# Kernel optimization log

Measured on AMD Instinct MI355X. Metric: run time of the kernel, lower is better.

## Reference

```python
import jax, jax.numpy as jnp
import numpy as np

B, C, H, W = 8, 21, 512, 512
MAX_M = 0.5   # args.ldam_max_m
S = 30.0      # args.ldam_s


def setup_inputs() -> dict:
    key = jax.random.key(0)
    k1, k2 = jax.random.split(key)
    pred = jax.random.normal(k1, (B, C, H, W), dtype=jnp.float32)
    target = jax.random.randint(k2, (B, H, W), 0, C, dtype=jnp.int32)  # class labels (argmax of one-hot)
    return {"pred": pred, "target": target}


def reference(pred, target):
    labels = target.reshape(-1)  # [N]
    # m_list: per-class pixel counts == sum of one-hot target over (0,2,3)
    counts = jnp.zeros((C,), dtype=pred.dtype).at[labels].add(1.0)
    m_list = 1.0 / jnp.sqrt(jnp.sqrt(counts + 1e-4))
    m_list = m_list * (MAX_M / jnp.max(m_list))

    logits = pred.transpose(0, 2, 3, 1).reshape(-1, C)  # [N, C]
    batch_m = m_list[labels]                            # gather == matmul(m_list, one_hot^T)
    onehot = jax.nn.one_hot(labels, C, dtype=logits.dtype)
    output = logits - batch_m[:, None] * onehot         # subtract margin only at target class

    logp = jax.nn.log_softmax(S * output, axis=-1)
    nll = -jnp.take_along_axis(logp, labels[:, None].astype(jnp.int32), axis=1)[:, 0]
    return jnp.mean(nll)
```

## Files before the change

### kernel.cpp

```cpp
#include <hip/hip_runtime.h>

static constexpr int   Cc  = 21;
static constexpr int   HWn = 512 * 512;
static constexpr int   Nn  = 8 * HWn;
static constexpr float MAXM  = 0.5f;
static constexpr float Sc    = 30.0f;
static constexpr float LOG2E = 1.4426950408889634f;
static constexpr float LN2   = 0.6931471805599453f;

static constexpr int HIST_BLOCKS = 512;
static constexpr int LOSS_BLOCKS = Nn / 4 / 256;

static constexpr int WS_COUNTS = 0;
static constexpr int WS_FLAG   = 96;
static constexpr int WS_PART   = 128;

__global__ __launch_bounds__(256) void hist_kernel(const int4* __restrict__ t4,
                                                   int* __restrict__ counts) {
    __shared__ int lh[4][Cc];
    int t = threadIdx.x;
    if (t < 4 * Cc) ((int*)lh)[t] = 0;
    __syncthreads();
    int wave = t >> 6;
    int base = blockIdx.x * (256 * 4) + t;
    #pragma unroll
    for (int i = 0; i < 4; ++i) {
        int4 v = t4[base + i * 256];
        atomicAdd(&lh[wave][v.x], 1);
        atomicAdd(&lh[wave][v.y], 1);
        atomicAdd(&lh[wave][v.z], 1);
        atomicAdd(&lh[wave][v.w], 1);
    }
    __syncthreads();
    if (t < Cc)
        atomicAdd(&counts[t], lh[0][t] + lh[1][t] + lh[2][t] + lh[3][t]);
}

__global__ __launch_bounds__(256, 4) void loss_kernel(const float* __restrict__ pred,
                                                      const int4* __restrict__ t4,
                                                      const int* __restrict__ counts,
                                                      double* __restrict__ partial,
                                                      unsigned int* __restrict__ flag,
                                                      float* __restrict__ out) {
    __shared__ double wsum[4];
    __shared__ bool   s_last;
    int t    = threadIdx.x;
    int lane = t & 63;

    float mval = 0.0f;
    if (lane < Cc) {
        float cnt = (float)counts[lane] + 1e-4f;
        mval = 1.0f / sqrtf(sqrtf(cnt));
    }
    float mxm = mval;
    #pragma unroll
    for (int o = 32; o >= 1; o >>= 1) mxm = fmaxf(mxm, __shfl_down(mxm, o));
    mxm = __shfl(mxm, 0);
    float smv = Sc * LOG2E * mval * (MAXM / mxm);

    int tid = blockIdx.x * 256 + t;
    int n0  = tid * 4;
    int b   = n0 >> 18;
    int hw  = n0 & (HWn - 1);
    const float4* p4 = (const float4*)(pred + (size_t)b * Cc * HWn + hw);

    int4 y4 = t4[tid];
    int ys[4] = {y4.x, y4.y, y4.z, y4.w};
    float smy[4];
    #pragma unroll
    for (int k = 0; k < 4; ++k) smy[k] = __shfl(smv, ys[k]);

    const float S2 = Sc * LOG2E;
    float m[4], s[4], vy[4];
    #pragma unroll
    for (int k = 0; k < 4; ++k) { m[k] = -1e30f; s[k] = 0.0f; vy[k] = 0.0f; }

    #pragma unroll
    for (int c = 0; c < Cc; ++c) {
        float4 xc = p4[(size_t)c * (HWn / 4)];
        float xs[4] = {xc.x, xc.y, xc.z, xc.w};
        #pragma unroll
        for (int k = 0; k < 4; ++k) {
            bool  isy = (c == ys[k]);
            float val = fmaf(S2, xs[k], isy ? -smy[k] : 0.0f);
            float mn  = fmaxf(m[k], val);
            s[k]  = fmaf(s[k], exp2f(m[k] - mn), exp2f(val - mn));
            m[k]  = mn;
            vy[k] = isy ? val : vy[k];
        }
    }

    float nll = 0.0f;
    #pragma unroll
    for (int k = 0; k < 4; ++k) nll += __log2f(s[k]) + m[k] - vy[k];
    nll *= LN2;

    #pragma unroll
    for (int o = 32; o >= 1; o >>= 1) nll += __shfl_down(nll, o);

    int wave = t >> 6;
    if ((t & 63) == 0) wsum[wave] = (double)nll;
    __syncthreads();
    if (t == 0) {
        double bsum = wsum[0] + wsum[1] + wsum[2] + wsum[3];
        partial[blockIdx.x] = bsum;
        __threadfence();
        unsigned done = atomicAdd(flag, 1u);
        s_last = (done == (unsigned)(LOSS_BLOCKS - 1));
    }
    __syncthreads();

    if (s_last) {
        __threadfence();
        double sm = 0.0;
        for (int i = t; i < LOSS_BLOCKS; i += 256) sm += partial[i];
        #pragma unroll
        for (int o = 32; o >= 1; o >>= 1) sm += __shfl_down(sm, o);
        if ((t & 63) == 0) wsum[t >> 6] = sm;
        __syncthreads();
        if (t == 0)
            out[0] = (float)((wsum[0] + wsum[1] + wsum[2] + wsum[3]) / (double)Nn);
    }
}

extern "C" void kernel_launch(void* const* d_in, const int* in_sizes, int n_in,
                              void* d_out, int out_size, void* d_ws, size_t ws_size,
                              hipStream_t stream) {
    const float* pred   = (const float*)d_in[0];
    const int*   target = (const int*)d_in[1];
    float*       out    = (float*)d_out;

    char* ws = (char*)d_ws;
    int*          counts  = (int*)(ws + WS_COUNTS);
    unsigned int* flag    = (unsigned int*)(ws + WS_FLAG);
    double*       partial = (double*)(ws + WS_PART);

    hipMemsetAsync(d_ws, 0, 128, stream);

    hist_kernel <<<HIST_BLOCKS, 256, 0, stream>>>((const int4*)target, counts);
    loss_kernel <<<LOSS_BLOCKS, 256, 0, stream>>>(pred, (const int4*)target,
                                                  counts, partial, flag, out);
}
```

Baseline: 339.9 us.

## Use two-pass softmax with one pixel per thread and grid-stride loop

Replaces the online softmax over four pixels per thread with a two-pass max-then-sum softmax on one pixel per thread, holding all 21 class logits in registers. The grid becomes a fixed 2048 blocks, each thread looping four times over strided chunks, with launch bounds raised to 6 blocks per SM. This removes the per-class rescaling exponentials of the online method and cuts the partials reduced at the end. The cost is scalar 4-byte loads in place of float4 loads, and more register pressure from keeping 21 values live.

Measured after the change: 353.5 us. 4.0% more time.

```diff
diff --git a/kernel.cpp b/kernel.cpp
--- a/kernel.cpp
+++ b/kernel.cpp
@@ -9,7 +9,9 @@
 static constexpr float LN2   = 0.6931471805599453f;
 
 static constexpr int HIST_BLOCKS = 512;
-static constexpr int LOSS_BLOCKS = Nn / 4 / 256;
+static constexpr int LOSS_BLOCKS = 2048;
+static constexpr int LOSS_ITERS  = 4;
+static constexpr int CHUNK       = Nn / LOSS_ITERS;
 
 static constexpr int WS_COUNTS = 0;
 static constexpr int WS_FLAG   = 96;
@@ -36,8 +38,8 @@
         atomicAdd(&counts[t], lh[0][t] + lh[1][t] + lh[2][t] + lh[3][t]);
 }
 
-__global__ __launch_bounds__(256, 4) void loss_kernel(const float* __restrict__ pred,
-                                                      const int4* __restrict__ t4,
+__global__ __launch_bounds__(256, 6) void loss_kernel(const float* __restrict__ pred,
+                                                      const int* __restrict__ target,
                                                       const int* __restrict__ counts,
                                                       double* __restrict__ partial,
                                                       unsigned int* __restrict__ flag,
@@ -58,42 +60,42 @@
     mxm = __shfl(mxm, 0);
     float smv = Sc * LOG2E * mval * (MAXM / mxm);
 
+    const float S2 = Sc * LOG2E;
     int tid = blockIdx.x * 256 + t;
-    int n0  = tid * 4;
-    int b   = n0 >> 18;
-    int hw  = n0 & (HWn - 1);
-    const float4* p4 = (const float4*)(pred + (size_t)b * Cc * HWn + hw);
+    float nll2 = 0.0f;
 
-    int4 y4 = t4[tid];
-    int ys[4] = {y4.x, y4.y, y4.z, y4.w};
-    float smy[4];
-    #pragma unroll
-    for (int k = 0; k < 4; ++k) smy[k] = __shfl(smv, ys[k]);
+    #pragma unroll 1
+    for (int it = 0; it < LOSS_ITERS; ++it) {
+        int n  = tid + it * CHUNK;
+        int b  = n >> 18;
+        int hw = n & (HWn - 1);
+        const float* p = pred + (size_t)b * (Cc * HWn) + hw;
 
-    const float S2 = Sc * LOG2E;
-    float m[4], s[4], vy[4];
-    #pragma unroll
-    for (int k = 0; k < 4; ++k) { m[k] = -1e30f; s[k] = 0.0f; vy[k] = 0.0f; }
+        float x[Cc];
+        #pragma unroll
+        for (int c = 0; c < Cc; ++c) x[c] = p[c * HWn];
 
-    #pragma unroll
-    for (int c = 0; c < Cc; ++c) {
-        float4 xc = p4[(size_t)c * (HWn / 4)];
-        float xs[4] = {xc.x, xc.y, xc.z, xc.w};
+        int   y   = target[n];
+        float smy = __shfl(smv, y);
+
+        float mx = -1e30f, vy = 0.0f;
         #pragma unroll
-        for (int k = 0; k < 4; ++k) {
-            bool  isy = (c == ys[k]);
-            float val = fmaf(S2, xs[k], isy ? -smy[k] : 0.0f);
-            float mn  = fmaxf(m[k], val);
-            s[k]  = fmaf(s[k], exp2f(m[k] - mn), exp2f(val - mn));
-            m[k]  = mn;
-            vy[k] = isy ? val : vy[k];
+        for (int c = 0; c < Cc; ++c) {
+            bool  isy = (c == y);
+            float val = fmaf(S2, x[c], isy ? -smy : 0.0f);
+            mx = fmaxf(mx, val);
+            vy = isy ? val : vy;
         }
+
+        float cb = -mx, cy = -smy - mx;
+        float sum = 0.0f;
+        #pragma unroll
+        for (int c = 0; c < Cc; ++c)
+            sum += exp2f(fmaf(S2, x[c], (c == y) ? cy : cb));
+
+        nll2 += __log2f(sum) + mx - vy;
     }
-
-    float nll = 0.0f;
-    #pragma unroll
-    for (int k = 0; k < 4; ++k) nll += __log2f(s[k]) + m[k] - vy[k];
-    nll *= LN2;
+    float nll = nll2 * LN2;
 
     #pragma unroll
     for (int o = 32; o >= 1; o >>= 1) nll += __shfl_down(nll, o);
@@ -138,6 +140,6 @@
     hipMemsetAsync(d_ws, 0, 128, stream);
 
     hist_kernel <<<HIST_BLOCKS, 256, 0, stream>>>((const int4*)target, counts);
-    loss_kernel <<<LOSS_BLOCKS, 256, 0, stream>>>(pred, (const int4*)target,
+    loss_kernel <<<LOSS_BLOCKS, 256, 0, stream>>>(pred, target,
                                                   counts, partial, flag, out);
 }
```

## Preload all class logits into registers and use two-pass softmax

Applied to the files above, without the earlier changes.

All 21 float4 class loads are issued up front, before the margin computation, and pinned in registers with an empty asm barrier so their latency overlaps the count/shuffle work. The online softmax is replaced by a max pass followed by a sum-of-exp2 pass, which drops the extra rescale exp per element. To fit the 84 live floats per thread, the launch bound is lowered from 4 to 2 blocks per SM, which trades occupancy for memory-level parallelism.

New measurement: 380.0 us. 1.12x slower.

```diff
diff --git a/kernel.cpp b/kernel.cpp
--- a/kernel.cpp
+++ b/kernel.cpp
@@ -36,7 +36,7 @@
         atomicAdd(&counts[t], lh[0][t] + lh[1][t] + lh[2][t] + lh[3][t]);
 }
 
-__global__ __launch_bounds__(256, 4) void loss_kernel(const float* __restrict__ pred,
+__global__ __launch_bounds__(256, 2) void loss_kernel(const float* __restrict__ pred,
                                                       const int4* __restrict__ t4,
                                                       const int* __restrict__ counts,
                                                       double* __restrict__ partial,
@@ -46,6 +46,22 @@
     __shared__ bool   s_last;
     int t    = threadIdx.x;
     int lane = t & 63;
+
+    int tid = blockIdx.x * 256 + t;
+    int n0  = tid * 4;
+    int b   = n0 >> 18;
+    int hw  = n0 & (HWn - 1);
+    const float4* p4 = (const float4*)(pred + (size_t)b * Cc * HWn + hw);
+
+    float4 x[Cc];
+    #pragma unroll
+    for (int c = 0; c < Cc; ++c) x[c] = p4[(size_t)c * (HWn / 4)];
+
+    #pragma unroll
+    for (int c = 0; c < Cc; ++c)
+        asm volatile("" : "+v"(x[c].x), "+v"(x[c].y), "+v"(x[c].z), "+v"(x[c].w));
+
+    int4 y4 = t4[tid];
 
     float mval = 0.0f;
     if (lane < Cc) {
@@ -58,42 +74,41 @@
     mxm = __shfl(mxm, 0);
     float smv = Sc * LOG2E * mval * (MAXM / mxm);
 
-    int tid = blockIdx.x * 256 + t;
-    int n0  = tid * 4;
-    int b   = n0 >> 18;
-    int hw  = n0 & (HWn - 1);
-    const float4* p4 = (const float4*)(pred + (size_t)b * Cc * HWn + hw);
-
-    int4 y4 = t4[tid];
     int ys[4] = {y4.x, y4.y, y4.z, y4.w};
     float smy[4];
     #pragma unroll
     for (int k = 0; k < 4; ++k) smy[k] = __shfl(smv, ys[k]);
 
     const float S2 = Sc * LOG2E;
-    float m[4], s[4], vy[4];
-    #pragma unroll
-    for (int k = 0; k < 4; ++k) { m[k] = -1e30f; s[k] = 0.0f; vy[k] = 0.0f; }
 
+    float mx[4] = {-1e30f, -1e30f, -1e30f, -1e30f};
+    float vy[4] = {0.f, 0.f, 0.f, 0.f};
     #pragma unroll
     for (int c = 0; c < Cc; ++c) {
-        float4 xc = p4[(size_t)c * (HWn / 4)];
-        float xs[4] = {xc.x, xc.y, xc.z, xc.w};
+        float xs[4] = {x[c].x, x[c].y, x[c].z, x[c].w};
         #pragma unroll
         for (int k = 0; k < 4; ++k) {
             bool  isy = (c == ys[k]);
             float val = fmaf(S2, xs[k], isy ? -smy[k] : 0.0f);
-            float mn  = fmaxf(m[k], val);
-            s[k]  = fmaf(s[k], exp2f(m[k] - mn), exp2f(val - mn));
-            m[k]  = mn;
+            mx[k] = fmaxf(mx[k], val);
             vy[k] = isy ? val : vy[k];
         }
     }
 
-    float nll = 0.0f;
+    float nll2 = 0.0f;
     #pragma unroll
-    for (int k = 0; k < 4; ++k) nll += __log2f(s[k]) + m[k] - vy[k];
-    nll *= LN2;
+    for (int k = 0; k < 4; ++k) {
+        float cb = -mx[k];
+        float cy = -smy[k] - mx[k];
+        float sum = 0.0f;
+        #pragma unroll
+        for (int c = 0; c < Cc; ++c) {
+            float xs = (k == 0) ? x[c].x : (k == 1) ? x[c].y : (k == 2) ? x[c].z : x[c].w;
+            sum += exp2f(fmaf(S2, xs, (c == ys[k]) ? cy : cb));
+        }
+        nll2 += __log2f(sum) + mx[k] - vy[k];
+    }
+    float nll = nll2 * LN2;
 
     #pragma unroll
     for (int o = 32; o >= 1; o >>= 1) nll += __shfl_down(nll, o);
```
